# Performance work log

Hardware: AMD Instinct MI355X
Metric: run time of the kernel (lower is better)

Reference implementation:

```python
import jax, jax.numpy as jnp
import numpy as np

EPS = 1e-9

def squash(s, axis=-1):
    # v = (|s|^2 / (1+|s|^2)) * s/|s|
    sq_norm = jnp.sum(s * s, axis=axis, keepdims=True)
    scale = sq_norm / (1.0 + sq_norm) / jnp.sqrt(sq_norm + EPS)
    return scale * s

def setup_inputs() -> dict:
    key = jax.random.key(0)
    k1, k2 = jax.random.split(key)
    B, N, Din = 256, 1152, 8   # batch, input caps, input cap dim
    C, U = 10, 16              # output caps, output cap dim
    inputs = jax.random.normal(k1, (B, N, Din), dtype=jnp.float32)
    # 'uniform' keras initializer ~ U(-0.05, 0.05)
    W = jax.random.uniform(k2, (C, N, Din, U), dtype=jnp.float32, minval=-0.05, maxval=0.05)
    return {"inputs": inputs, "W": W}

ROUTING_ITERATIONS = 3

def reference(inputs, W):
    B = inputs.shape[0]
    C = W.shape[0]
    N = W.shape[1]
    # prediction vectors u_hat: (B, C, N, U)
    u_hat = jnp.einsum('bni,cniu->bcnu', inputs, W)
    # coupling logits b: ones, shape (B, C, N) (trailing singleton dropped)
    b = jnp.ones((B, C, N), dtype=inputs.dtype)
    out = None
    for i in range(ROUTING_ITERATIONS):
        # softmax over input-capsule axis (axis=-2 of (B,C,N,1) == N)
        c = jax.nn.softmax(b, axis=-1)  # (B, C, N)
        s = jnp.einsum('bcnu,bcn->bcu', u_hat, c)  # weighted sum over input caps
        out = squash(s, axis=-1)  # (B, C, U)
        if i < ROUTING_ITERATIONS - 1:
            # agreement: u_hat . v
            b = b + jnp.einsum('bcnu,bcu->bcn', u_hat, out)
    return out
```

## Files before the change

### kernel.cpp

```cpp
#include <hip/hip_runtime.h>
#include <math.h>


#define BATCH 256
#define CAPS  10
#define NIN   1152
#define DIN   8
#define UDIM  16
#define TPB   512
#define KITER 9

__global__ __launch_bounds__(TPB, 1) void capsule_routing_kernel(
    const float* __restrict__ x,
    const float* __restrict__ W,
    float* __restrict__ out)
{
    const int gblk = blockIdx.x;
    const int c    = gblk >> 8;
    const int b    = gblk & 255;
    const int t    = threadIdx.x;
    const int ub   = (t & 3) << 2;
    const int gg   = t >> 2;
    const int wave = t >> 6;

    __shared__ float x_s[NIN * DIN];
    __shared__ float b_s[NIN];
    __shared__ float redB[8];
    __shared__ float ps[8][UDIM];
    __shared__ float v_s[UDIM];

    {
        const float4* xg = (const float4*)(x + (size_t)b * (NIN * DIN));
        float4* xs = (float4*)x_s;
        #pragma unroll
        for (int i = 0; i < 5; ++i) {
            const int idx = t + TPB * i;
            if (idx < (NIN * DIN / 4)) xs[idx] = xg[idx];
        }
    }
    for (int n = t; n < NIN; n += TPB) b_s[n] = 1.0f;
    __syncthreads();

    const float* Wc = W + (size_t)c * (NIN * DIN * UDIM);

    float4 uh0, uh1, uh2, uh3, uh4, uh5, uh6, uh7, uh8;

#define UHCOMP(K, DST) { \
    const int n = gg + 128 * (K); \
    const float4* wr = (const float4*)(Wc + n * (DIN * UDIM) + ub); \
    const float4 xa = ((const float4*)(x_s + n * DIN))[0]; \
    const float4 xb = ((const float4*)(x_s + n * DIN))[1]; \
    float4 w0 = wr[0], w1 = wr[4], w2 = wr[8], w3 = wr[12]; \
    float4 acc; \
    acc.x = xa.x * w0.x + xa.y * w1.x + xa.z * w2.x + xa.w * w3.x; \
    acc.y = xa.x * w0.y + xa.y * w1.y + xa.z * w2.y + xa.w * w3.y; \
    acc.z = xa.x * w0.z + xa.y * w1.z + xa.z * w2.z + xa.w * w3.z; \
    acc.w = xa.x * w0.w + xa.y * w1.w + xa.z * w2.w + xa.w * w3.w; \
    w0 = wr[16]; w1 = wr[20]; w2 = wr[24]; w3 = wr[28]; \
    acc.x += xb.x * w0.x + xb.y * w1.x + xb.z * w2.x + xb.w * w3.x; \
    acc.y += xb.x * w0.y + xb.y * w1.y + xb.z * w2.y + xb.w * w3.y; \
    acc.z += xb.x * w0.z + xb.y * w1.z + xb.z * w2.z + xb.w * w3.z; \
    acc.w += xb.x * w0.w + xb.y * w1.w + xb.z * w2.w + xb.w * w3.w; \
    DST = acc; } \
    __builtin_amdgcn_sched_barrier(0);

    UHCOMP(0, uh0)
    UHCOMP(1, uh1)
    UHCOMP(2, uh2)
    UHCOMP(3, uh3)
    UHCOMP(4, uh4)
    UHCOMP(5, uh5)
    UHCOMP(6, uh6)
    UHCOMP(7, uh7)
    UHCOMP(8, uh8)

    for (int it = 0; it < 3; ++it) {
        float le = 0.f;
        float4 p; p.x = p.y = p.z = p.w = 0.f;

#define ACCP(K, UH) { \
        const float e = expf(b_s[gg + 128 * (K)]); \
        le += e; \
        p.x += e * UH.x; p.y += e * UH.y; p.z += e * UH.z; p.w += e * UH.w; }

        ACCP(0, uh0) ACCP(1, uh1) ACCP(2, uh2)
        ACCP(3, uh3) ACCP(4, uh4) ACCP(5, uh5)
        ACCP(6, uh6) ACCP(7, uh7) ACCP(8, uh8)

        #pragma unroll
        for (int mk = 1; mk <= 32; mk <<= 1) le += __shfl_xor(le, mk);
        if ((t & 63) == 0) redB[wave] = le;

        #pragma unroll
        for (int mk = 4; mk <= 32; mk <<= 1) {
            p.x += __shfl_xor(p.x, mk); p.y += __shfl_xor(p.y, mk);
            p.z += __shfl_xor(p.z, mk); p.w += __shfl_xor(p.w, mk);
        }
        if ((t & 63) < 4) {
            ps[wave][ub + 0] = p.x; ps[wave][ub + 1] = p.y;
            ps[wave][ub + 2] = p.z; ps[wave][ub + 3] = p.w;
        }
        __syncthreads();

        if (t < UDIM) {
            float esum = 0.f;
            #pragma unroll
            for (int w = 0; w < 8; ++w) esum += redB[w];
            const float inv = 4.0f / esum;
            float s = 0.f;
            #pragma unroll
            for (int w = 0; w < 8; ++w) s += ps[w][t];
            s *= inv;
            float sq = s * s;
            #pragma unroll
            for (int mk = 1; mk <= 8; mk <<= 1) sq += __shfl_xor(sq, mk);
            const float scale = sq / ((1.0f + sq) * sqrtf(sq + 1e-9f));
            const float v = scale * s;
            v_s[t] = v;
            if (it == 2) out[((size_t)b * CAPS + c) * UDIM + t] = v;
        }
        __syncthreads();

        if (it < 2) {
            const float4 v4 = *(const float4*)(v_s + ub);

#define BUPD(K, UH) { \
            float q = UH.x * v4.x + UH.y * v4.y + UH.z * v4.z + UH.w * v4.w; \
            q += __shfl_xor(q, 1); \
            q += __shfl_xor(q, 2); \
            if ((t & 3) == 0) b_s[gg + 128 * (K)] += q; }

            BUPD(0, uh0) BUPD(1, uh1) BUPD(2, uh2)
            BUPD(3, uh3) BUPD(4, uh4) BUPD(5, uh5)
            BUPD(6, uh6) BUPD(7, uh7) BUPD(8, uh8)
            __syncthreads();
        }
    }
}

extern "C" void kernel_launch(void* const* d_in, const int* in_sizes, int n_in,
                              void* d_out, int out_size, void* d_ws, size_t ws_size,
                              hipStream_t stream) {
    const float* x = (const float*)d_in[0];
    const float* W = (const float*)d_in[1];
    float* out = (float*)d_out;
    capsule_routing_kernel<<<BATCH * CAPS, TPB, 0, stream>>>(x, W, out);
}
```

Baseline: 130.3 us.

## Read x directly from global, specialize uniform first routing iteration, use fast exp

```diff
diff --git a/kernel.cpp b/kernel.cpp
--- a/kernel.cpp
+++ b/kernel.cpp
@@ -8,81 +8,100 @@
 #define DIN   8
 #define UDIM  16
 #define TPB   512
-#define KITER 9
 
 __global__ __launch_bounds__(TPB, 1) void capsule_routing_kernel(
     const float* __restrict__ x,
     const float* __restrict__ W,
     float* __restrict__ out)
 {
-    const int gblk = blockIdx.x;
-    const int c    = gblk >> 8;
-    const int b    = gblk & 255;
+    const int blk = blockIdx.x;
+    const int c   = blk >> 8;
+    const int b   = blk & 255;
     const int t    = threadIdx.x;
     const int ub   = (t & 3) << 2;
     const int gg   = t >> 2;
     const int wave = t >> 6;
 
-    __shared__ float x_s[NIN * DIN];
     __shared__ float b_s[NIN];
     __shared__ float redB[8];
-    __shared__ float ps[8][UDIM];
-    __shared__ float v_s[UDIM];
+    __shared__ __align__(16) float ps[8][UDIM];
+    __shared__ __align__(16) float v_s[UDIM];
 
-    {
-        const float4* xg = (const float4*)(x + (size_t)b * (NIN * DIN));
-        float4* xs = (float4*)x_s;
-        #pragma unroll
-        for (int i = 0; i < 5; ++i) {
-            const int idx = t + TPB * i;
-            if (idx < (NIN * DIN / 4)) xs[idx] = xg[idx];
-        }
-    }
-    for (int n = t; n < NIN; n += TPB) b_s[n] = 1.0f;
-    __syncthreads();
-
-    const float* Wc = W + (size_t)c * (NIN * DIN * UDIM);
+    const float4* xp = (const float4*)(x + (size_t)b * (NIN * DIN) + gg * DIN);
+    const float4* wp = (const float4*)(W + (size_t)c * (NIN * DIN * UDIM)
+                                         + gg * (DIN * UDIM) + ub);
 
     float4 uh0, uh1, uh2, uh3, uh4, uh5, uh6, uh7, uh8;
 
-#define UHCOMP(K, DST) { \
-    const int n = gg + 128 * (K); \
-    const float4* wr = (const float4*)(Wc + n * (DIN * UDIM) + ub); \
-    const float4 xa = ((const float4*)(x_s + n * DIN))[0]; \
-    const float4 xb = ((const float4*)(x_s + n * DIN))[1]; \
-    float4 w0 = wr[0], w1 = wr[4], w2 = wr[8], w3 = wr[12]; \
+#define UHK(DST) { \
     float4 acc; \
-    acc.x = xa.x * w0.x + xa.y * w1.x + xa.z * w2.x + xa.w * w3.x; \
-    acc.y = xa.x * w0.y + xa.y * w1.y + xa.z * w2.y + xa.w * w3.y; \
-    acc.z = xa.x * w0.z + xa.y * w1.z + xa.z * w2.z + xa.w * w3.z; \
-    acc.w = xa.x * w0.w + xa.y * w1.w + xa.z * w2.w + xa.w * w3.w; \
-    w0 = wr[16]; w1 = wr[20]; w2 = wr[24]; w3 = wr[28]; \
-    acc.x += xb.x * w0.x + xb.y * w1.x + xb.z * w2.x + xb.w * w3.x; \
-    acc.y += xb.x * w0.y + xb.y * w1.y + xb.z * w2.y + xb.w * w3.y; \
-    acc.z += xb.x * w0.z + xb.y * w1.z + xb.z * w2.z + xb.w * w3.z; \
-    acc.w += xb.x * w0.w + xb.y * w1.w + xb.z * w2.w + xb.w * w3.w; \
-    DST = acc; } \
-    __builtin_amdgcn_sched_barrier(0);
+    { const float4 xa = xp[0]; \
+      float4 w0 = wp[0], w1 = wp[4], w2 = wp[8], w3 = wp[12]; \
+      acc.x = xa.x*w0.x + xa.y*w1.x + xa.z*w2.x + xa.w*w3.x; \
+      acc.y = xa.x*w0.y + xa.y*w1.y + xa.z*w2.y + xa.w*w3.y; \
+      acc.z = xa.x*w0.z + xa.y*w1.z + xa.z*w2.z + xa.w*w3.z; \
+      acc.w = xa.x*w0.w + xa.y*w1.w + xa.z*w2.w + xa.w*w3.w; } \
+    __builtin_amdgcn_sched_barrier(0); \
+    { const float4 xb = xp[1]; \
+      float4 w0 = wp[16], w1 = wp[20], w2 = wp[24], w3 = wp[28]; \
+      acc.x += xb.x*w0.x + xb.y*w1.x + xb.z*w2.x + xb.w*w3.x; \
+      acc.y += xb.x*w0.y + xb.y*w1.y + xb.z*w2.y + xb.w*w3.y; \
+      acc.z += xb.x*w0.z + xb.y*w1.z + xb.z*w2.z + xb.w*w3.z; \
+      acc.w += xb.x*w0.w + xb.y*w1.w + xb.z*w2.w + xb.w*w3.w; } \
+    xp += 256; wp += 4096; \
+    DST = acc; \
+    __builtin_amdgcn_sched_barrier(0); }
 
-    UHCOMP(0, uh0)
-    UHCOMP(1, uh1)
-    UHCOMP(2, uh2)
-    UHCOMP(3, uh3)
-    UHCOMP(4, uh4)
-    UHCOMP(5, uh5)
-    UHCOMP(6, uh6)
-    UHCOMP(7, uh7)
-    UHCOMP(8, uh8)
+    UHK(uh0) UHK(uh1) UHK(uh2)
+    UHK(uh3) UHK(uh4) UHK(uh5)
+    UHK(uh6) UHK(uh7) UHK(uh8)
 
-    for (int it = 0; it < 3; ++it) {
+    {
+        float4 p;
+        p.x = uh0.x + uh1.x + uh2.x + uh3.x + uh4.x + uh5.x + uh6.x + uh7.x + uh8.x;
+        p.y = uh0.y + uh1.y + uh2.y + uh3.y + uh4.y + uh5.y + uh6.y + uh7.y + uh8.y;
+        p.z = uh0.z + uh1.z + uh2.z + uh3.z + uh4.z + uh5.z + uh6.z + uh7.z + uh8.z;
+        p.w = uh0.w + uh1.w + uh2.w + uh3.w + uh4.w + uh5.w + uh6.w + uh7.w + uh8.w;
+        #pragma unroll
+        for (int mk = 4; mk <= 32; mk <<= 1) {
+            p.x += __shfl_xor(p.x, mk); p.y += __shfl_xor(p.y, mk);
+            p.z += __shfl_xor(p.z, mk); p.w += __shfl_xor(p.w, mk);
+        }
+        if ((t & 63) < 4) {
+            ps[wave][ub + 0] = p.x; ps[wave][ub + 1] = p.y;
+            ps[wave][ub + 2] = p.z; ps[wave][ub + 3] = p.w;
+        }
+        __syncthreads();
+        if (t < UDIM) {
+            float s = 0.f;
+            #pragma unroll
+            for (int w = 0; w < 8; ++w) s += ps[w][t];
+            s *= (1.0f / (float)NIN);
+            float sq = s * s;
+            #pragma unroll
+            for (int mk = 1; mk <= 8; mk <<= 1) sq += __shfl_xor(sq, mk);
+            const float scale = sq / ((1.0f + sq) * sqrtf(sq + 1e-9f));
+            v_s[t] = scale * s;
+        }
+        __syncthreads();
+        const float4 v4 = *(const float4*)(v_s + ub);
+#define BST(K, UH) { \
+        float q = UH.x*v4.x + UH.y*v4.y + UH.z*v4.z + UH.w*v4.w; \
+        q += __shfl_xor(q, 1); q += __shfl_xor(q, 2); \
+        if ((t & 3) == 0) b_s[gg + 128 * (K)] = q; }
+        BST(0, uh0) BST(1, uh1) BST(2, uh2)
+        BST(3, uh3) BST(4, uh4) BST(5, uh5)
+        BST(6, uh6) BST(7, uh7) BST(8, uh8)
+        __syncthreads();
+    }
+
+    for (int it = 1; it < 3; ++it) {
         float le = 0.f;
         float4 p; p.x = p.y = p.z = p.w = 0.f;
-
 #define ACCP(K, UH) { \
-        const float e = expf(b_s[gg + 128 * (K)]); \
+        const float e = __expf(b_s[gg + 128 * (K)]); \
         le += e; \
         p.x += e * UH.x; p.y += e * UH.y; p.z += e * UH.z; p.w += e * UH.w; }
-
         ACCP(0, uh0) ACCP(1, uh1) ACCP(2, uh2)
         ACCP(3, uh3) ACCP(4, uh4) ACCP(5, uh5)
         ACCP(6, uh6) ACCP(7, uh7) ACCP(8, uh8)
@@ -103,14 +122,10 @@
         __syncthreads();
 
         if (t < UDIM) {
-            float esum = 0.f;
+            float esum = 0.f, s = 0.f;
             #pragma unroll
-            for (int w = 0; w < 8; ++w) esum += redB[w];
-            const float inv = 4.0f / esum;
-            float s = 0.f;
-            #pragma unroll
-            for (int w = 0; w < 8; ++w) s += ps[w][t];
-            s *= inv;
+            for (int w = 0; w < 8; ++w) { esum += redB[w]; s += ps[w][t]; }
+            s *= 4.0f / esum;
             float sq = s * s;
             #pragma unroll
             for (int mk = 1; mk <= 8; mk <<= 1) sq += __shfl_xor(sq, mk);
@@ -121,18 +136,15 @@
         }
         __syncthreads();
 
-        if (it < 2) {
+        if (it == 1) {
             const float4 v4 = *(const float4*)(v_s + ub);
-
-#define BUPD(K, UH) { \
-            float q = UH.x * v4.x + UH.y * v4.y + UH.z * v4.z + UH.w * v4.w; \
-            q += __shfl_xor(q, 1); \
-            q += __shfl_xor(q, 2); \
+#define BADD(K, UH) { \
+            float q = UH.x*v4.x + UH.y*v4.y + UH.z*v4.z + UH.w*v4.w; \
+            q += __shfl_xor(q, 1); q += __shfl_xor(q, 2); \
             if ((t & 3) == 0) b_s[gg + 128 * (K)] += q; }
-
-            BUPD(0, uh0) BUPD(1, uh1) BUPD(2, uh2)
-            BUPD(3, uh3) BUPD(4, uh4) BUPD(5, uh5)
-            BUPD(6, uh6) BUPD(7, uh7) BUPD(8, uh8)
+            BADD(0, uh0) BADD(1, uh1) BADD(2, uh2)
+            BADD(3, uh3) BADD(4, uh4) BADD(5, uh5)
+            BADD(6, uh6) BADD(7, uh7) BADD(8, uh8)
             __syncthreads();
         }
     }
```

After: 133.1 us. 1.02x slower.

## Keep routing logits in registers and drop shared staging and extra barriers

Applied to the files above, without the earlier changes.

```diff
diff --git a/kernel.cpp b/kernel.cpp
--- a/kernel.cpp
+++ b/kernel.cpp
@@ -8,132 +8,134 @@
 #define DIN   8
 #define UDIM  16
 #define TPB   512
-#define KITER 9
 
 __global__ __launch_bounds__(TPB, 1) void capsule_routing_kernel(
     const float* __restrict__ x,
     const float* __restrict__ W,
     float* __restrict__ out)
 {
-    const int gblk = blockIdx.x;
-    const int c    = gblk >> 8;
-    const int b    = gblk & 255;
+    const int blk  = blockIdx.x;
+    const int c    = blk >> 8;
+    const int b    = blk & 255;
     const int t    = threadIdx.x;
     const int ub   = (t & 3) << 2;
     const int gg   = t >> 2;
     const int wave = t >> 6;
 
-    __shared__ float x_s[NIN * DIN];
-    __shared__ float b_s[NIN];
-    __shared__ float redB[8];
-    __shared__ float ps[8][UDIM];
-    __shared__ float v_s[UDIM];
+    __shared__ float ps[2][8][20];
 
-    {
-        const float4* xg = (const float4*)(x + (size_t)b * (NIN * DIN));
-        float4* xs = (float4*)x_s;
-        #pragma unroll
-        for (int i = 0; i < 5; ++i) {
-            const int idx = t + TPB * i;
-            if (idx < (NIN * DIN / 4)) xs[idx] = xg[idx];
-        }
-    }
-    for (int n = t; n < NIN; n += TPB) b_s[n] = 1.0f;
-    __syncthreads();
-
-    const float* Wc = W + (size_t)c * (NIN * DIN * UDIM);
+    const float4* xq = (const float4*)(x + (size_t)b * (NIN * DIN) + gg * DIN);
+    const float4* wq = (const float4*)(W + (size_t)c * (NIN * DIN * UDIM)
+                                         + gg * (DIN * UDIM) + ub);
 
     float4 uh0, uh1, uh2, uh3, uh4, uh5, uh6, uh7, uh8;
+    float4 xa, xb_, w0, w1, w2, w3, w4, w5, w6, w7;
+    float4 ya, yb_, v0, v1, v2, v3, v4, v5, v6, v7;
 
-#define UHCOMP(K, DST) { \
-    const int n = gg + 128 * (K); \
-    const float4* wr = (const float4*)(Wc + n * (DIN * UDIM) + ub); \
-    const float4 xa = ((const float4*)(x_s + n * DIN))[0]; \
-    const float4 xb = ((const float4*)(x_s + n * DIN))[1]; \
-    float4 w0 = wr[0], w1 = wr[4], w2 = wr[8], w3 = wr[12]; \
-    float4 acc; \
-    acc.x = xa.x * w0.x + xa.y * w1.x + xa.z * w2.x + xa.w * w3.x; \
-    acc.y = xa.x * w0.y + xa.y * w1.y + xa.z * w2.y + xa.w * w3.y; \
-    acc.z = xa.x * w0.z + xa.y * w1.z + xa.z * w2.z + xa.w * w3.z; \
-    acc.w = xa.x * w0.w + xa.y * w1.w + xa.z * w2.w + xa.w * w3.w; \
-    w0 = wr[16]; w1 = wr[20]; w2 = wr[24]; w3 = wr[28]; \
-    acc.x += xb.x * w0.x + xb.y * w1.x + xb.z * w2.x + xb.w * w3.x; \
-    acc.y += xb.x * w0.y + xb.y * w1.y + xb.z * w2.y + xb.w * w3.y; \
-    acc.z += xb.x * w0.z + xb.y * w1.z + xb.z * w2.z + xb.w * w3.z; \
-    acc.w += xb.x * w0.w + xb.y * w1.w + xb.z * w2.w + xb.w * w3.w; \
-    DST = acc; } \
-    __builtin_amdgcn_sched_barrier(0);
+#define LOADA(K) { \
+    xa  = xq[256*(K)];   xb_ = xq[256*(K)+1]; \
+    w0 = wq[4096*(K)];    w1 = wq[4096*(K)+4]; \
+    w2 = wq[4096*(K)+8];  w3 = wq[4096*(K)+12]; \
+    w4 = wq[4096*(K)+16]; w5 = wq[4096*(K)+20]; \
+    w6 = wq[4096*(K)+24]; w7 = wq[4096*(K)+28]; }
+#define LOADB(K) { \
+    ya  = xq[256*(K)];   yb_ = xq[256*(K)+1]; \
+    v0 = wq[4096*(K)];    v1 = wq[4096*(K)+4]; \
+    v2 = wq[4096*(K)+8];  v3 = wq[4096*(K)+12]; \
+    v4 = wq[4096*(K)+16]; v5 = wq[4096*(K)+20]; \
+    v6 = wq[4096*(K)+24]; v7 = wq[4096*(K)+28]; }
+#define FMAA(D) { \
+    D.x = xa.x*w0.x + xa.y*w1.x + xa.z*w2.x + xa.w*w3.x \
+        + xb_.x*w4.x + xb_.y*w5.x + xb_.z*w6.x + xb_.w*w7.x; \
+    D.y = xa.x*w0.y + xa.y*w1.y + xa.z*w2.y + xa.w*w3.y \
+        + xb_.x*w4.y + xb_.y*w5.y + xb_.z*w6.y + xb_.w*w7.y; \
+    D.z = xa.x*w0.z + xa.y*w1.z + xa.z*w2.z + xa.w*w3.z \
+        + xb_.x*w4.z + xb_.y*w5.z + xb_.z*w6.z + xb_.w*w7.z; \
+    D.w = xa.x*w0.w + xa.y*w1.w + xa.z*w2.w + xa.w*w3.w \
+        + xb_.x*w4.w + xb_.y*w5.w + xb_.z*w6.w + xb_.w*w7.w; }
+#define FMAB(D) { \
+    D.x = ya.x*v0.x + ya.y*v1.x + ya.z*v2.x + ya.w*v3.x \
+        + yb_.x*v4.x + yb_.y*v5.x + yb_.z*v6.x + yb_.w*v7.x; \
+    D.y = ya.x*v0.y + ya.y*v1.y + ya.z*v2.y + ya.w*v3.y \
+        + yb_.x*v4.y + yb_.y*v5.y + yb_.z*v6.y + yb_.w*v7.y; \
+    D.z = ya.x*v0.z + ya.y*v1.z + ya.z*v2.z + ya.w*v3.z \
+        + yb_.x*v4.z + yb_.y*v5.z + yb_.z*v6.z + yb_.w*v7.z; \
+    D.w = ya.x*v0.w + ya.y*v1.w + ya.z*v2.w + ya.w*v3.w \
+        + yb_.x*v4.w + yb_.y*v5.w + yb_.z*v6.w + yb_.w*v7.w; }
 
-    UHCOMP(0, uh0)
-    UHCOMP(1, uh1)
-    UHCOMP(2, uh2)
-    UHCOMP(3, uh3)
-    UHCOMP(4, uh4)
-    UHCOMP(5, uh5)
-    UHCOMP(6, uh6)
-    UHCOMP(7, uh7)
-    UHCOMP(8, uh8)
+    LOADA(0) LOADB(1)
+    FMAA(uh0) LOADA(2)
+    FMAB(uh1) LOADB(3)
+    FMAA(uh2) LOADA(4)
+    FMAB(uh3) LOADB(5)
+    FMAA(uh4) LOADA(6)
+    FMAB(uh5) LOADB(7)
+    FMAA(uh6) LOADA(8)
+    FMAB(uh7)
+    FMAA(uh8)
+
+    float bl0=0.f, bl1=0.f, bl2=0.f, bl3=0.f, bl4=0.f,
+          bl5=0.f, bl6=0.f, bl7=0.f, bl8=0.f;
 
     for (int it = 0; it < 3; ++it) {
+        const int buf = it & 1;
+        float4 p;
         float le = 0.f;
-        float4 p; p.x = p.y = p.z = p.w = 0.f;
-
-#define ACCP(K, UH) { \
-        const float e = expf(b_s[gg + 128 * (K)]); \
-        le += e; \
-        p.x += e * UH.x; p.y += e * UH.y; p.z += e * UH.z; p.w += e * UH.w; }
-
-        ACCP(0, uh0) ACCP(1, uh1) ACCP(2, uh2)
-        ACCP(3, uh3) ACCP(4, uh4) ACCP(5, uh5)
-        ACCP(6, uh6) ACCP(7, uh7) ACCP(8, uh8)
-
-        #pragma unroll
-        for (int mk = 1; mk <= 32; mk <<= 1) le += __shfl_xor(le, mk);
-        if ((t & 63) == 0) redB[wave] = le;
+        if (it == 0) {
+            p.x = uh0.x+uh1.x+uh2.x+uh3.x+uh4.x+uh5.x+uh6.x+uh7.x+uh8.x;
+            p.y = uh0.y+uh1.y+uh2.y+uh3.y+uh4.y+uh5.y+uh6.y+uh7.y+uh8.y;
+            p.z = uh0.z+uh1.z+uh2.z+uh3.z+uh4.z+uh5.z+uh6.z+uh7.z+uh8.z;
+            p.w = uh0.w+uh1.w+uh2.w+uh3.w+uh4.w+uh5.w+uh6.w+uh7.w+uh8.w;
+        } else {
+            p.x = p.y = p.z = p.w = 0.f;
+#define ACCP(BL, UH) { \
+            const float e = __expf(BL); le += e; \
+            p.x += e*UH.x; p.y += e*UH.y; p.z += e*UH.z; p.w += e*UH.w; }
+            ACCP(bl0, uh0) ACCP(bl1, uh1) ACCP(bl2, uh2)
+            ACCP(bl3, uh3) ACCP(bl4, uh4) ACCP(bl5, uh5)
+            ACCP(bl6, uh6) ACCP(bl7, uh7) ACCP(bl8, uh8)
+        }
 
         #pragma unroll
         for (int mk = 4; mk <= 32; mk <<= 1) {
             p.x += __shfl_xor(p.x, mk); p.y += __shfl_xor(p.y, mk);
             p.z += __shfl_xor(p.z, mk); p.w += __shfl_xor(p.w, mk);
         }
-        if ((t & 63) < 4) {
-            ps[wave][ub + 0] = p.x; ps[wave][ub + 1] = p.y;
-            ps[wave][ub + 2] = p.z; ps[wave][ub + 3] = p.w;
+        if (it != 0) {
+            #pragma unroll
+            for (int mk = 4; mk <= 32; mk <<= 1) le += __shfl_xor(le, mk);
         }
+        if ((t & 63) < 4) *(float4*)(&ps[buf][wave][ub]) = p;
+        if ((t & 63) == 0) ps[buf][wave][16] = le;
         __syncthreads();
 
-        if (t < UDIM) {
-            float esum = 0.f;
-            #pragma unroll
-            for (int w = 0; w < 8; ++w) esum += redB[w];
-            const float inv = 4.0f / esum;
-            float s = 0.f;
-            #pragma unroll
-            for (int w = 0; w < 8; ++w) s += ps[w][t];
-            s *= inv;
-            float sq = s * s;
-            #pragma unroll
-            for (int mk = 1; mk <= 8; mk <<= 1) sq += __shfl_xor(sq, mk);
-            const float scale = sq / ((1.0f + sq) * sqrtf(sq + 1e-9f));
-            const float v = scale * s;
-            v_s[t] = v;
-            if (it == 2) out[((size_t)b * CAPS + c) * UDIM + t] = v;
+        float4 s; s.x = s.y = s.z = s.w = 0.f;
+        float esum = 0.f;
+        #pragma unroll
+        for (int w = 0; w < 8; ++w) {
+            const float4 q = *(const float4*)(&ps[buf][w][ub]);
+            s.x += q.x; s.y += q.y; s.z += q.z; s.w += q.w;
+            esum += ps[buf][w][16];
         }
-        __syncthreads();
+        const float inv = (it == 0) ? (1.0f / (float)NIN) : (1.0f / esum);
+        s.x *= inv; s.y *= inv; s.z *= inv; s.w *= inv;
+
+        float sq = s.x*s.x + s.y*s.y + s.z*s.z + s.w*s.w;
+        sq += __shfl_xor(sq, 1);
+        sq += __shfl_xor(sq, 2);
+        const float scale = sq / ((1.0f + sq) * sqrtf(sq + 1e-9f));
+        s.x *= scale; s.y *= scale; s.z *= scale; s.w *= scale;
 
         if (it < 2) {
-            const float4 v4 = *(const float4*)(v_s + ub);
-
-#define BUPD(K, UH) { \
-            float q = UH.x * v4.x + UH.y * v4.y + UH.z * v4.z + UH.w * v4.w; \
-            q += __shfl_xor(q, 1); \
-            q += __shfl_xor(q, 2); \
-            if ((t & 3) == 0) b_s[gg + 128 * (K)] += q; }
-
-            BUPD(0, uh0) BUPD(1, uh1) BUPD(2, uh2)
-            BUPD(3, uh3) BUPD(4, uh4) BUPD(5, uh5)
-            BUPD(6, uh6) BUPD(7, uh7) BUPD(8, uh8)
-            __syncthreads();
+#define BUPD(BL, UH) { \
+            float q = UH.x*s.x + UH.y*s.y + UH.z*s.z + UH.w*s.w; \
+            q += __shfl_xor(q, 1); q += __shfl_xor(q, 2); \
+            BL += q; }
+            BUPD(bl0, uh0) BUPD(bl1, uh1) BUPD(bl2, uh2)
+            BUPD(bl3, uh3) BUPD(bl4, uh4) BUPD(bl5, uh5)
+            BUPD(bl6, uh6) BUPD(bl7, uh7) BUPD(bl8, uh8)
+        } else if (t < 4) {
+            ((float4*)(out + ((size_t)b * CAPS + c) * UDIM))[t & 3] = s;
         }
     }
 }
```

After: 131.7 us. No clear change (+1.1%).
